# Performance work log

Measured on AMD Instinct MI355X. Metric: run time of the kernel, lower is better.

The kernel has to match this reference:

```python
import jax, jax.numpy as jnp
import numpy as np

N, K, D = 8192, 4096, 256


def setup_inputs() -> dict:
    key = jax.random.key(0)
    kx, kc, kw = jax.random.split(key, 3)
    x = jax.random.normal(kx, (N, D), dtype=jnp.float32)
    centers = jax.random.normal(kc, (K, D), dtype=jnp.float32)
    w = jax.random.normal(kw, (K,), dtype=jnp.float32)
    # bandwidth chosen so exp(-sigma * d2) stays in a healthy range for
    # Gaussian data where E[||x-c||^2] ~= 2*D
    sigma = jnp.asarray(1.0 / (2.0 * D), dtype=jnp.float32)
    return {"x": x, "centers": centers, "w": w, "sigma": sigma}


def reference(x, centers, w, sigma):
    # phi[n,k] = exp(-sigma * ||x_n - c_k||^2), computed via the GEMM
    x2 = jnp.sum(x * x, axis=-1, keepdims=True)          # [N,1]
    c2 = jnp.sum(centers * centers, axis=-1)             # [K]
    d2 = x2 + c2 - 2.0 * jnp.einsum('nd,kd->nk', x, centers)  # [N,K]
    d2 = jnp.maximum(d2, 0.0)  # clamp tiny negative round-off
    phi = jnp.exp(-sigma * d2)                           # [N,K]
    # (w * phi).sum(1) == phi @ w
    return jnp.einsum('nk,k->n', phi, w)                 # [N]
```

## Files before the change

kernel.cpp:

```cpp
#include <hip/hip_runtime.h>

#define NROWS 8192
#define NCENT 4096
#define DIM   256

typedef short bf16x8 __attribute__((ext_vector_type(8)));
typedef float f32x4  __attribute__((ext_vector_type(4)));

__device__ inline unsigned short f2bf(float f) {
    unsigned u = __float_as_uint(f);
    return (unsigned short)((u + 0x7fffu + ((u >> 16) & 1u)) >> 16);
}

__global__ __launch_bounds__(256) void norms_kernel(const float* __restrict__ x,
                                                    const float* __restrict__ c,
                                                    float* __restrict__ ws) {
    int t = threadIdx.x, lane = t & 63;
    int gw = blockIdx.x * 4 + (t >> 6);
    const float* src;
    float* dst;
    if (gw < NROWS) { src = x + (size_t)gw * DIM;           dst = ws + gw; }
    else            { src = c + (size_t)(gw - NROWS) * DIM; dst = ws + gw; }
    float4 v = ((const float4*)src)[lane];
    float s = v.x * v.x + v.y * v.y + v.z * v.z + v.w * v.w;
    #pragma unroll
    for (int m = 32; m; m >>= 1) s += __shfl_xor(s, m);
    if (lane == 0) *dst = s;
}

__global__ __launch_bounds__(256) void pack_kernel(const float* __restrict__ x,
                                                   const float* __restrict__ c,
                                                   unsigned short* __restrict__ xp,
                                                   unsigned short* __restrict__ cp) {
    const int t = threadIdx.x, lane = t & 63;
    const int task = blockIdx.x * 4 + (t >> 6);
    const int lr = lane & 15, g = lane >> 4;
    const float* src;
    unsigned short* dst;
    int tg, ks;
    if (task < (NROWS / 16) * 8) {
        tg = task >> 3; ks = task & 7;
        src = x;  dst = xp + (size_t)task * 512;
    } else {
        int tk = task - (NROWS / 16) * 8;
        tg = tk >> 3; ks = tk & 7;
        src = c;  dst = cp + (size_t)tk * 512;
    }
    const float* p = src + (size_t)(tg * 16 + lr) * DIM + ks * 32 + g * 8;
    float4 f0 = *(const float4*)p;
    float4 f1 = *(const float4*)(p + 4);
    union { unsigned short s[8]; int4 v; } u;
    u.s[0] = f2bf(f0.x); u.s[1] = f2bf(f0.y); u.s[2] = f2bf(f0.z); u.s[3] = f2bf(f0.w);
    u.s[4] = f2bf(f1.x); u.s[5] = f2bf(f1.y); u.s[6] = f2bf(f1.z); u.s[7] = f2bf(f1.w);
    *(int4*)(dst + lane * 8) = u.v;
}

__global__ __launch_bounds__(64, 2) void rbf_mfma(const unsigned short* __restrict__ xp,
                                                  const unsigned short* __restrict__ cp,
                                                  const float* __restrict__ w,
                                                  const float* __restrict__ sigp,
                                                  const float* __restrict__ norms,
                                                  float* __restrict__ out) {
    const int lane = threadIdx.x;
    const int lr = lane & 15, g = lane >> 4;

    const int lin = blockIdx.x;
    const int xcd = lin & 7;
    const int pos = lin >> 3;
    const int mi  = xcd * 16 + (pos >> 5);
    const int ni  = pos & 31;
    const int m0  = mi * 64;
    const int n0  = ni * 128;

    const unsigned short* pa[4];
    const unsigned short* pb[8];
    #pragma unroll
    for (int i = 0; i < 4; ++i)
        pa[i] = xp + ((size_t)((m0 >> 4) + i) * 8) * 512 + lane * 8;
    #pragma unroll
    for (int j = 0; j < 8; ++j)
        pb[j] = cp + ((size_t)((n0 >> 4) + j) * 8) * 512 + lane * 8;

    f32x4 acc[4][8];
    #pragma unroll
    for (int i = 0; i < 4; ++i)
        #pragma unroll
        for (int j = 0; j < 8; ++j) acc[i][j] = f32x4{0, 0, 0, 0};

    bf16x8 a[4], b[8], an[4], bn[8];
    #pragma unroll
    for (int i = 0; i < 4; ++i) a[i] = *(const bf16x8*)(pa[i]);
    #pragma unroll
    for (int j = 0; j < 8; ++j) b[j] = *(const bf16x8*)(pb[j]);

    #pragma unroll
    for (int s = 0; s < 8; ++s) {
        if (s < 7) {
            #pragma unroll
            for (int i = 0; i < 4; ++i) an[i] = *(const bf16x8*)(pa[i] + (s + 1) * 512);
            #pragma unroll
            for (int j = 0; j < 8; ++j) bn[j] = *(const bf16x8*)(pb[j] + (s + 1) * 512);
        }
        #pragma unroll
        for (int i = 0; i < 4; ++i)
            #pragma unroll
            for (int j = 0; j < 8; ++j)
                acc[i][j] = __builtin_amdgcn_mfma_f32_16x16x32_bf16(a[i], b[j], acc[i][j], 0, 0, 0);
        #pragma unroll
        for (int i = 0; i < 4; ++i) a[i] = an[i];
        #pragma unroll
        for (int j = 0; j < 8; ++j) b[j] = bn[j];
    }

    const float sigma = sigp[0];
    float c2v[8], wv[8];
    #pragma unroll
    for (int j = 0; j < 8; ++j) {
        int n = n0 + 16 * j + lr;
        c2v[j] = norms[NROWS + n];
        wv[j]  = w[n];
    }

    #pragma unroll
    for (int i = 0; i < 4; ++i) {
        const int mbase = m0 + 16 * i + 4 * g;
        float4 x2v = *(const float4*)(norms + mbase);
        float rs[4] = {0.f, 0.f, 0.f, 0.f};
        #pragma unroll
        for (int j = 0; j < 8; ++j) {
            #pragma unroll
            for (int r = 0; r < 4; ++r) {
                float x2r = (r == 0) ? x2v.x : (r == 1) ? x2v.y : (r == 2) ? x2v.z : x2v.w;
                float d2 = x2r + c2v[j] - 2.0f * acc[i][j][r];
                d2 = fmaxf(d2, 0.0f);
                rs[r] += wv[j] * __expf(-sigma * d2);
            }
        }
        #pragma unroll
        for (int r = 0; r < 4; ++r) {
            rs[r] += __shfl_xor(rs[r], 1);
            rs[r] += __shfl_xor(rs[r], 2);
            rs[r] += __shfl_xor(rs[r], 4);
            rs[r] += __shfl_xor(rs[r], 8);
        }
        if (lr == 0) {
            #pragma unroll
            for (int r = 0; r < 4; ++r) atomicAdd(&out[mbase + r], rs[r]);
        }
    }
}

__global__ __launch_bounds__(256) void rbf_kernel(const float* __restrict__ x,
                                                  const float* __restrict__ cent,
                                                  const float* __restrict__ w,
                                                  const float* __restrict__ sigp,
                                                  const float* __restrict__ norms,
                                                  float* __restrict__ out) {
    __shared__ __align__(16) short xs[64 * 32];
    __shared__ __align__(16) short cs[64 * 32];
    const int t = threadIdx.x;
    const int m0 = blockIdx.y * 64, n0 = blockIdx.x * 64;
    const int srow = t >> 2, seg = t & 3;
    const int pchunk = seg ^ ((srow >> 1) & 3);
    const int sidx = srow * 32 + pchunk * 8;
    const float* xg = x    + (size_t)(m0 + srow) * DIM + seg * 8;
    const float* cg = cent + (size_t)(n0 + srow) * DIM + seg * 8;
    const int lane = t & 63, wave = t >> 6;
    const int lr = lane & 15, lg = lane >> 4;
    const int arow = 16 * wave + lr;
    const int aidx = arow * 32 + ((lg ^ ((arow >> 1) & 3)) * 8);
    f32x4 acc[4] = {f32x4{0,0,0,0}, f32x4{0,0,0,0}, f32x4{0,0,0,0}, f32x4{0,0,0,0}};
    for (int k0 = 0; k0 < DIM; k0 += 32) {
        float4 f0 = *(const float4*)(xg + k0);
        float4 f1 = *(const float4*)(xg + k0 + 4);
        float4 g0 = *(const float4*)(cg + k0);
        float4 g1 = *(const float4*)(cg + k0 + 4);
        __syncthreads();
        union { unsigned short s[8]; int4 v; } ux, uc;
        ux.s[0]=f2bf(f0.x); ux.s[1]=f2bf(f0.y); ux.s[2]=f2bf(f0.z); ux.s[3]=f2bf(f0.w);
        ux.s[4]=f2bf(f1.x); ux.s[5]=f2bf(f1.y); ux.s[6]=f2bf(f1.z); ux.s[7]=f2bf(f1.w);
        uc.s[0]=f2bf(g0.x); uc.s[1]=f2bf(g0.y); uc.s[2]=f2bf(g0.z); uc.s[3]=f2bf(g0.w);
        uc.s[4]=f2bf(g1.x); uc.s[5]=f2bf(g1.y); uc.s[6]=f2bf(g1.z); uc.s[7]=f2bf(g1.w);
        *(int4*)(xs + sidx) = ux.v;
        *(int4*)(cs + sidx) = uc.v;
        __syncthreads();
        bf16x8 a = *(const bf16x8*)(xs + aidx);
        #pragma unroll
        for (int bt = 0; bt < 4; ++bt) {
            const int brow = 16 * bt + lr;
            bf16x8 b = *(const bf16x8*)(cs + brow * 32 + ((lg ^ ((brow >> 1) & 3)) * 8));
            acc[bt] = __builtin_amdgcn_mfma_f32_16x16x32_bf16(a, b, acc[bt], 0, 0, 0);
        }
    }
    const float sigma = sigp[0];
    const int rbase = m0 + 16 * wave + lg * 4;
    float x2v[4];
    #pragma unroll
    for (int r = 0; r < 4; ++r) x2v[r] = norms[rbase + r];
    float rs[4] = {0.f, 0.f, 0.f, 0.f};
    #pragma unroll
    for (int bt = 0; bt < 4; ++bt) {
        const int col = n0 + 16 * bt + lr;
        const float c2v = norms[NROWS + col];
        const float wvv = w[col];
        #pragma unroll
        for (int r = 0; r < 4; ++r) {
            float d2 = x2v[r] + c2v - 2.0f * acc[bt][r];
            d2 = fmaxf(d2, 0.0f);
            rs[r] += wvv * __expf(-sigma * d2);
        }
    }
    #pragma unroll
    for (int r = 0; r < 4; ++r) {
        rs[r] += __shfl_xor(rs[r], 1);
        rs[r] += __shfl_xor(rs[r], 2);
        rs[r] += __shfl_xor(rs[r], 4);
        rs[r] += __shfl_xor(rs[r], 8);
    }
    if (lr == 0) {
        #pragma unroll
        for (int r = 0; r < 4; ++r) atomicAdd(&out[rbase + r], rs[r]);
    }
}

extern "C" void kernel_launch(void* const* d_in, const int* in_sizes, int n_in,
                              void* d_out, int out_size, void* d_ws, size_t ws_size,
                              hipStream_t stream) {
    const float* x    = (const float*)d_in[0];
    const float* cent = (const float*)d_in[1];
    const float* w    = (const float*)d_in[2];
    const float* sig  = (const float*)d_in[3];
    float* out = (float*)d_out;

    const size_t norms_elems = NROWS + NCENT;
    const size_t xp_off  = norms_elems * sizeof(float);
    const size_t cp_off  = xp_off + (size_t)NROWS * DIM * sizeof(unsigned short);
    const size_t ws_need = cp_off + (size_t)NCENT * DIM * sizeof(unsigned short);

    hipMemsetAsync(d_out, 0, (size_t)out_size * sizeof(float), stream);
    float* norms = (float*)d_ws;
    norms_kernel<<<(NROWS + NCENT) / 4, 256, 0, stream>>>(x, cent, norms);

    if (ws_size >= ws_need) {
        unsigned short* xp = (unsigned short*)((char*)d_ws + xp_off);
        unsigned short* cp = (unsigned short*)((char*)d_ws + cp_off);
        pack_kernel<<<((NROWS + NCENT) / 16 * 8) / 4, 256, 0, stream>>>(x, cent, xp, cp);
        rbf_mfma<<<(NROWS / 64) * (NCENT / 128), 64, 0, stream>>>(xp, cp, w, sig, norms, out);
    } else {
        rbf_kernel<<<dim3(NCENT / 64, NROWS / 64), 256, 0, stream>>>(x, cent, w, sig, norms, out);
    }
}
```

Baseline: 110.5 us.

## Keep A tile resident in registers and stream center tiles with fused epilogue

The MFMA kernel now loads the full 64x256 x tile into registers once and walks 256 centers in 16-column chunks. Each chunk's bf16 MFMA result is turned straight into a weighted exp and accumulated into per-row sums, with double-buffered prefetch of the next chunk's B fragments. This halves the block count and the number of atomics per output row, and it folds sigma into the norms so the epilogue becomes an fma plus fmin. The cost is heavy register use (32 A fragments plus two B buffers), which may reduce occupancy or cause spills.

Measured after the change: 205.8 us. +86.2%, slower.

```diff
diff --git a/kernel.cpp b/kernel.cpp
--- a/kernel.cpp
+++ b/kernel.cpp
@@ -55,99 +55,118 @@
     *(int4*)(dst + lane * 8) = u.v;
 }
 
-__global__ __launch_bounds__(64, 2) void rbf_mfma(const unsigned short* __restrict__ xp,
-                                                  const unsigned short* __restrict__ cp,
-                                                  const float* __restrict__ w,
-                                                  const float* __restrict__ sigp,
-                                                  const float* __restrict__ norms,
-                                                  float* __restrict__ out) {
+__global__ __launch_bounds__(64, 2) void rbf_stream(const unsigned short* __restrict__ xp,
+                                                    const unsigned short* __restrict__ cp,
+                                                    const float* __restrict__ w,
+                                                    const float* __restrict__ sigp,
+                                                    const float* __restrict__ norms,
+                                                    float* __restrict__ out) {
     const int lane = threadIdx.x;
     const int lr = lane & 15, g = lane >> 4;
 
     const int lin = blockIdx.x;
     const int xcd = lin & 7;
     const int pos = lin >> 3;
-    const int mi  = xcd * 16 + (pos >> 5);
-    const int ni  = pos & 31;
-    const int m0  = mi * 64;
-    const int n0  = ni * 128;
-
-    const unsigned short* pa[4];
-    const unsigned short* pb[8];
+    const int m0  = (xcd * 16 + (pos >> 4)) * 64;
+    const int n0  = (pos & 15) * 256;
+
+    bf16x8 A[4][8];
+    {
+        const unsigned short* ap = xp + ((size_t)(m0 >> 4) * 8) * 512 + lane * 8;
+        #pragma unroll
+        for (int i = 0; i < 4; ++i)
+            #pragma unroll
+            for (int s = 0; s < 8; ++s)
+                A[i][s] = *(const bf16x8*)(ap + (size_t)(i * 8 + s) * 512);
+    }
+
+    const float K = -sigp[0];
+    const float M = -2.0f * K;
+    float kx2[4][4];
+    #pragma unroll
+    for (int i = 0; i < 4; ++i) {
+        float4 v = *(const float4*)(norms + m0 + 16 * i + 4 * g);
+        kx2[i][0] = K * v.x; kx2[i][1] = K * v.y;
+        kx2[i][2] = K * v.z; kx2[i][3] = K * v.w;
+    }
+
+    float sums[4][4];
     #pragma unroll
     for (int i = 0; i < 4; ++i)
-        pa[i] = xp + ((size_t)((m0 >> 4) + i) * 8) * 512 + lane * 8;
-    #pragma unroll
-    for (int j = 0; j < 8; ++j)
-        pb[j] = cp + ((size_t)((n0 >> 4) + j) * 8) * 512 + lane * 8;
-
-    f32x4 acc[4][8];
+        #pragma unroll
+        for (int r = 0; r < 4; ++r) sums[i][r] = 0.f;
+
+    const unsigned short* bp = cp + ((size_t)(n0 >> 4) * 8) * 512 + lane * 8;
+
+    bf16x8 B0[8], B1[8];
+    #pragma unroll
+    for (int s = 0; s < 8; ++s) B0[s] = *(const bf16x8*)(bp + s * 512);
+    #pragma unroll
+    for (int s = 0; s < 8; ++s) B1[s] = *(const bf16x8*)(bp + 4096 + s * 512);
+
+    #pragma unroll
+    for (int c = 0; c < 16; c += 2) {
+        {
+            f32x4 acc[4] = {f32x4{0,0,0,0}, f32x4{0,0,0,0}, f32x4{0,0,0,0}, f32x4{0,0,0,0}};
+            #pragma unroll
+            for (int s = 0; s < 8; ++s)
+                #pragma unroll
+                for (int i = 0; i < 4; ++i)
+                    acc[i] = __builtin_amdgcn_mfma_f32_16x16x32_bf16(A[i][s], B0[s], acc[i], 0, 0, 0);
+            if (c + 2 < 16) {
+                #pragma unroll
+                for (int s = 0; s < 8; ++s)
+                    B0[s] = *(const bf16x8*)(bp + (size_t)(c + 2) * 4096 + s * 512);
+            }
+            const int col = n0 + 16 * c + lr;
+            const float kc2 = K * norms[NROWS + col];
+            const float wv  = w[col];
+            #pragma unroll
+            for (int i = 0; i < 4; ++i)
+                #pragma unroll
+                for (int r = 0; r < 4; ++r) {
+                    float t = fmaf(M, acc[i][r], kx2[i][r] + kc2);
+                    t = fminf(t, 0.0f);
+                    sums[i][r] = fmaf(wv, __expf(t), sums[i][r]);
+                }
+        }
+        {
+            f32x4 acc[4] = {f32x4{0,0,0,0}, f32x4{0,0,0,0}, f32x4{0,0,0,0}, f32x4{0,0,0,0}};
+            #pragma unroll
+            for (int s = 0; s < 8; ++s)
+                #pragma unroll
+                for (int i = 0; i < 4; ++i)
+                    acc[i] = __builtin_amdgcn_mfma_f32_16x16x32_bf16(A[i][s], B1[s], acc[i], 0, 0, 0);
+            if (c + 3 < 16) {
+                #pragma unroll
+                for (int s = 0; s < 8; ++s)
+                    B1[s] = *(const bf16x8*)(bp + (size_t)(c + 3) * 4096 + s * 512);
+            }
+            const int col = n0 + 16 * (c + 1) + lr;
+            const float kc2 = K * norms[NROWS + col];
+            const float wv  = w[col];
+            #pragma unroll
+            for (int i = 0; i < 4; ++i)
+                #pragma unroll
+                for (int r = 0; r < 4; ++r) {
+                    float t = fmaf(M, acc[i][r], kx2[i][r] + kc2);
+                    t = fminf(t, 0.0f);
+                    sums[i][r] = fmaf(wv, __expf(t), sums[i][r]);
+                }
+        }
+    }
+
     #pragma unroll
     for (int i = 0; i < 4; ++i)
         #pragma unroll
-        for (int j = 0; j < 8; ++j) acc[i][j] = f32x4{0, 0, 0, 0};
-
-    bf16x8 a[4], b[8], an[4], bn[8];
-    #pragma unroll
-    for (int i = 0; i < 4; ++i) a[i] = *(const bf16x8*)(pa[i]);
-    #pragma unroll
-    for (int j = 0; j < 8; ++j) b[j] = *(const bf16x8*)(pb[j]);
-
-    #pragma unroll
-    for (int s = 0; s < 8; ++s) {
-        if (s < 7) {
-            #pragma unroll
-            for (int i = 0; i < 4; ++i) an[i] = *(const bf16x8*)(pa[i] + (s + 1) * 512);
-            #pragma unroll
-            for (int j = 0; j < 8; ++j) bn[j] = *(const bf16x8*)(pb[j] + (s + 1) * 512);
-        }
-        #pragma unroll
-        for (int i = 0; i < 4; ++i)
-            #pragma unroll
-            for (int j = 0; j < 8; ++j)
-                acc[i][j] = __builtin_amdgcn_mfma_f32_16x16x32_bf16(a[i], b[j], acc[i][j], 0, 0, 0);
-        #pragma unroll
-        for (int i = 0; i < 4; ++i) a[i] = an[i];
-        #pragma unroll
-        for (int j = 0; j < 8; ++j) b[j] = bn[j];
-    }
-
-    const float sigma = sigp[0];
-    float c2v[8], wv[8];
-    #pragma unroll
-    for (int j = 0; j < 8; ++j) {
-        int n = n0 + 16 * j + lr;
-        c2v[j] = norms[NROWS + n];
-        wv[j]  = w[n];
-    }
-
-    #pragma unroll
-    for (int i = 0; i < 4; ++i) {
-        const int mbase = m0 + 16 * i + 4 * g;
-        float4 x2v = *(const float4*)(norms + mbase);
-        float rs[4] = {0.f, 0.f, 0.f, 0.f};
-        #pragma unroll
-        for (int j = 0; j < 8; ++j) {
-            #pragma unroll
-            for (int r = 0; r < 4; ++r) {
-                float x2r = (r == 0) ? x2v.x : (r == 1) ? x2v.y : (r == 2) ? x2v.z : x2v.w;
-                float d2 = x2r + c2v[j] - 2.0f * acc[i][j][r];
-                d2 = fmaxf(d2, 0.0f);
-                rs[r] += wv[j] * __expf(-sigma * d2);
-            }
-        }
-        #pragma unroll
         for (int r = 0; r < 4; ++r) {
-            rs[r] += __shfl_xor(rs[r], 1);
-            rs[r] += __shfl_xor(rs[r], 2);
-            rs[r] += __shfl_xor(rs[r], 4);
-            rs[r] += __shfl_xor(rs[r], 8);
-        }
-        if (lr == 0) {
-            #pragma unroll
-            for (int r = 0; r < 4; ++r) atomicAdd(&out[mbase + r], rs[r]);
-        }
-    }
+            float v = sums[i][r];
+            v += __shfl_xor(v, 1);
+            v += __shfl_xor(v, 2);
+            v += __shfl_xor(v, 4);
+            v += __shfl_xor(v, 8);
+            if (lr == 0) atomicAdd(&out[m0 + 16 * i + 4 * g + r], v);
+        }
 }
 
 __global__ __launch_bounds__(256) void rbf_kernel(const float* __restrict__ x,
@@ -245,7 +264,7 @@
         unsigned short* xp = (unsigned short*)((char*)d_ws + xp_off);
         unsigned short* cp = (unsigned short*)((char*)d_ws + cp_off);
         pack_kernel<<<((NROWS + NCENT) / 16 * 8) / 4, 256, 0, stream>>>(x, cent, xp, cp);
-        rbf_mfma<<<(NROWS / 64) * (NCENT / 128), 64, 0, stream>>>(xp, cp, w, sig, norms, out);
+        rbf_stream<<<2048, 64, 0, stream>>>(xp, cp, w, sig, norms, out);
     } else {
         rbf_kernel<<<dim3(NCENT / 64, NROWS / 64), 256, 0, stream>>>(x, cent, w, sig, norms, out);
     }
```
